# Kernel optimization log

Hardware: AMD Instinct MI355X
Metric: run time of the kernel (lower is better)

The kernel has to match this reference:

```python
import jax, jax.numpy as jnp
import numpy as np

TEMP = 0.07  # module hardcodes self.temp = 0.07 regardless of ctor arg
N, C = 8192, 256


def setup_inputs() -> dict:
    key = jax.random.key(0)
    kq, kk = jax.random.split(key)
    q = jax.random.normal(kq, (N, C), dtype=jnp.float32)
    k = jax.random.normal(kk, (N, C), dtype=jnp.float32)
    return {"q": q, "k": k}


def reference(q, k):
    # Original builds logits = [l_pos, l_neg_row] per sample i where
    # l_pos = q_i . k_i and l_neg_row = q_i . k_j for j != i, then applies
    # CrossEntropyLoss with label 0. That logits row is exactly a permutation
    # of the full similarity row sim[i, :] = q_i @ k.T (diagonal = positive),
    # so CE(logits/T, 0) == logsumexp(sim_i/T) - sim_ii/T. Single fused GEMM
    # + row-wise logsumexp, identical math and gradients.
    sim = jnp.matmul(q, k.T) / TEMP            # [N, N]
    pos = jnp.diagonal(sim)                    # [N]
    lse = jax.nn.logsumexp(sim, axis=1)        # [N]
    return jnp.mean(lse - pos)                 # scalar loss
```

## Files before the change

kernel.cpp:

```cpp
#include <hip/hip_runtime.h>
#include <stdint.h>


#define N_ROWS 8192
#define C_DIM  256
#define BN     64
#define SPLIT  16
#define JCOLS  (N_ROWS / SPLIT)
#define JTILES (JCOLS / BN)
#define RF     4
#define BLK_ROWS 256

typedef __attribute__((ext_vector_type(8))) _Float16 half8;
typedef __attribute__((ext_vector_type(4))) _Float16 half4;
typedef __attribute__((ext_vector_type(4))) float    f32x4;

#if __has_builtin(__builtin_amdgcn_exp2f)
#define EXP2(x) __builtin_amdgcn_exp2f(x)
#else
#define EXP2(x) exp2f(x)
#endif
#if __has_builtin(__builtin_amdgcn_logf)
#define LOG2(x) __builtin_amdgcn_logf(x)
#else
#define LOG2(x) log2f(x)
#endif

__device__ __forceinline__ void gload_lds16(const void* g, void* l) {
  __builtin_amdgcn_global_load_lds(
      (const __attribute__((address_space(1))) unsigned int*)g,
      (__attribute__((address_space(3))) unsigned int*)l, 16, 0, 0);
}

__global__ void cvt_kernel(const float* __restrict__ q, const float* __restrict__ k,
                           _Float16* __restrict__ qh, _Float16* __restrict__ kh,
                           float* __restrict__ pP) {
  const float QS = 20.60992915555663f;
  int i = blockIdx.x * 256 + threadIdx.x;
  float4 qv = ((const float4*)q)[i];
  float4 kv = ((const float4*)k)[i];
  half4 qo, ko;
  qo[0] = (_Float16)(qv.x * QS); qo[1] = (_Float16)(qv.y * QS);
  qo[2] = (_Float16)(qv.z * QS); qo[3] = (_Float16)(qv.w * QS);
  ko[0] = (_Float16)kv.x; ko[1] = (_Float16)kv.y;
  ko[2] = (_Float16)kv.z; ko[3] = (_Float16)kv.w;
  ((half4*)qh)[i] = qo;
  ((half4*)kh)[i] = ko;

  float d = (float)qo[0] * (float)ko[0];
  d = fmaf((float)qo[1], (float)ko[1], d);
  d = fmaf((float)qo[2], (float)ko[2], d);
  d = fmaf((float)qo[3], (float)ko[3], d);
#pragma unroll
  for (int off = 1; off < 64; off <<= 1) d += __shfl_xor(d, off);
  if ((threadIdx.x & 63) == 0) pP[i >> 6] = d;
}

__launch_bounds__(256, 2)
__global__ void sim_lse_kernel(const _Float16* __restrict__ qh,
                               const _Float16* __restrict__ kh,
                               float* __restrict__ pM,
                               float* __restrict__ pS) {
  __shared__ __align__(16) _Float16 kt[2 * BN * C_DIM];
  const int tid  = threadIdx.x;
  const int lane = tid & 63;
  const int wave = tid >> 6;
  const int l15  = lane & 15;
  const int lg   = lane >> 4;

  const int rb   = blockIdx.x;
  const int sp   = blockIdx.y;
  const int row0 = rb * BLK_ROWS + wave * 64;

  half8 a[RF][8];
#pragma unroll
  for (int rf = 0; rf < RF; ++rf) {
    const _Float16* qr = qh + (size_t)(row0 + rf * 16 + l15) * C_DIM + lg * 8;
#pragma unroll
    for (int f = 0; f < 8; ++f) a[rf][f] = *(const half8*)(qr + f * 32);
  }

  float M[RF][4], S[RF][4];
#pragma unroll
  for (int rf = 0; rf < RF; ++rf)
#pragma unroll
    for (int r = 0; r < 4; ++r) { M[rf][r] = -__builtin_inff(); S[rf][r] = 0.f; }

  int bbase[4];
#pragma unroll
  for (int cf = 0; cf < 4; ++cf) {
    int nl = cf * 16 + l15;
    bbase[cf] = nl * 512 + (((nl & 31) * 16) ^ (lg * 16));
  }

  const char* ksrc = (const char*)(kh + (size_t)sp * JCOLS * C_DIM);
  char* lds = (char*)kt;

#pragma unroll
  for (int it = 0; it < 8; ++it) {
    int linear = it * 4096 + tid * 16;
    int row = linear >> 9;
    int gc  = ((linear >> 4) & 31) ^ (row & 31);
    gload_lds16(ksrc + row * 512 + gc * 16, lds + linear);
  }

#pragma unroll 2
  for (int jt = 0; jt < JTILES; ++jt) {
    __syncthreads();
    const char* cur = lds + (jt & 1) * 32768;

    if (jt + 1 < JTILES) {
      const char* src = ksrc + (size_t)(jt + 1) * (BN * C_DIM * 2);
      char* nxt = lds + ((jt + 1) & 1) * 32768;
#pragma unroll
      for (int it = 0; it < 8; ++it) {
        int linear = it * 4096 + tid * 16;
        int row = linear >> 9;
        int gc  = ((linear >> 4) & 31) ^ (row & 31);
        gload_lds16(src + row * 512 + gc * 16, nxt + linear);
      }
    }

#pragma unroll
    for (int cp = 0; cp < 2; ++cp) {
      f32x4 acc0[RF], acc1[RF];
#pragma unroll
      for (int rf = 0; rf < RF; ++rf) {
        f32x4 z = {0.f, 0.f, 0.f, 0.f};
        acc0[rf] = z; acc1[rf] = z;
      }
      const int b0off = bbase[cp * 2];
      const int b1off = bbase[cp * 2 + 1];
#pragma unroll
      for (int ks = 0; ks < 8; ++ks) {
        half8 b0 = *(const half8*)(cur + (b0off ^ (ks * 64)));
        half8 b1 = *(const half8*)(cur + (b1off ^ (ks * 64)));
#pragma unroll
        for (int rf = 0; rf < RF; ++rf) {
          acc0[rf] = __builtin_amdgcn_mfma_f32_16x16x32_f16(a[rf][ks], b0, acc0[rf], 0, 0, 0);
          acc1[rf] = __builtin_amdgcn_mfma_f32_16x16x32_f16(a[rf][ks], b1, acc1[rf], 0, 0, 0);
        }
      }
#pragma unroll
      for (int rf = 0; rf < RF; ++rf)
#pragma unroll
        for (int r = 0; r < 4; ++r) {
          float v0 = acc0[rf][r], v1 = acc1[rf][r];
          float tmax  = fmaxf(v0, v1);
          float newM  = fmaxf(M[rf][r], tmax);
          float alpha = EXP2(M[rf][r] - newM);
          float p = EXP2(v0 - newM) + EXP2(v1 - newM);
          S[rf][r] = fmaf(S[rf][r], alpha, p);
          M[rf][r] = newM;
        }
    }
  }

#pragma unroll
  for (int rf = 0; rf < RF; ++rf)
#pragma unroll
    for (int r = 0; r < 4; ++r) {
#pragma unroll
      for (int off = 1; off < 16; off <<= 1) {
        float Mo = __shfl_xor(M[rf][r], off);
        float So = __shfl_xor(S[rf][r], off);
        float nm = fmaxf(M[rf][r], Mo);
        S[rf][r] = S[rf][r] * EXP2(M[rf][r] - nm) + So * EXP2(Mo - nm);
        M[rf][r] = nm;
      }
    }

  if (l15 == 0) {
#pragma unroll
    for (int rf = 0; rf < RF; ++rf)
#pragma unroll
      for (int r = 0; r < 4; ++r) {
        int grow = row0 + rf * 16 + lg * 4 + r;
        pM[(size_t)sp * N_ROWS + grow] = M[rf][r];
        pS[(size_t)sp * N_ROWS + grow] = S[rf][r];
      }
  }
}

__global__ void finish1_kernel(const float* __restrict__ pM, const float* __restrict__ pS,
                               const float* __restrict__ pP, float* __restrict__ pPart) {
  const int tid = threadIdx.x;
  const int r = blockIdx.x * 256 + tid;
  float m = -__builtin_inff();
#pragma unroll
  for (int s = 0; s < SPLIT; ++s) m = fmaxf(m, pM[s * N_ROWS + r]);
  float ssum = 0.f;
#pragma unroll
  for (int s = 0; s < SPLIT; ++s)
    ssum = fmaf(pS[s * N_ROWS + r], EXP2(pM[s * N_ROWS + r] - m), ssum);
  float accl = (m + LOG2(ssum)) - pP[r];
#pragma unroll
  for (int off = 1; off < 64; off <<= 1) accl += __shfl_xor(accl, off);
  __shared__ float wsum[4];
  if ((tid & 63) == 0) wsum[tid >> 6] = accl;
  __syncthreads();
  if (tid == 0)
    pPart[blockIdx.x] = wsum[0] + wsum[1] + wsum[2] + wsum[3];
}

__global__ void finish2_kernel(const float* __restrict__ pPart, float* __restrict__ out) {
  const int tid = threadIdx.x;
  float v = (tid < 32) ? pPart[tid] : 0.f;
#pragma unroll
  for (int off = 1; off < 64; off <<= 1) v += __shfl_xor(v, off);
  if (tid == 0)
    out[0] = v * (0.69314718055994531f / (float)N_ROWS);
}

extern "C" void kernel_launch(void* const* d_in, const int* in_sizes, int n_in,
                              void* d_out, int out_size, void* d_ws, size_t ws_size,
                              hipStream_t stream) {
  const float* q = (const float*)d_in[0];
  const float* k = (const float*)d_in[1];
  float* out = (float*)d_out;
  char* ws = (char*)d_ws;

  _Float16* qh = (_Float16*)ws;
  _Float16* kh = (_Float16*)(ws + (size_t)N_ROWS * C_DIM * 2);
  float* pM = (float*)(ws + (size_t)N_ROWS * C_DIM * 4);
  float* pS = pM + SPLIT * N_ROWS;
  float* pP = pS + SPLIT * N_ROWS;
  float* pPart = pP + N_ROWS;

  cvt_kernel<<<dim3(N_ROWS * C_DIM / 4 / 256), dim3(256), 0, stream>>>(q, k, qh, kh, pP);
  sim_lse_kernel<<<dim3(N_ROWS / BLK_ROWS, SPLIT), dim3(256), 0, stream>>>(qh, kh, pM, pS);
  finish1_kernel<<<dim3(N_ROWS / 256), dim3(256), 0, stream>>>(pM, pS, pP, pPart);
  finish2_kernel<<<dim3(1), dim3(64), 0, stream>>>(pPart, out);
}
```

Measured before the change: 137.9 us.

## Switch similarity GEMM to 32x32x16 MFMA with 128-row blocks and split 8

Replaces the 16x16x32 MFMA tiling (4 row fragments per wave, 64 rows) with 32x32x16 MFMA (32 rows per wave, 128-row blocks) and halves the column split from 16 to 8, flattening the grid to 1D with split as the fastest index. The goal is higher MFMA throughput per LDS read and fewer partial M/S results. The trade-off is less K-tile reuse per block (128 rows instead of 256), so the K matrix is re-read from global/LDS more often. Blocks sharing a row block are launched adjacently, which may help L2 locality. Row mapping for the 32x32 output layout is rewritten for the final stores.

```diff
diff --git a/kernel.cpp b/kernel.cpp
--- a/kernel.cpp
+++ b/kernel.cpp
@@ -5,15 +5,14 @@
 #define N_ROWS 8192
 #define C_DIM  256
 #define BN     64
-#define SPLIT  16
+#define SPLIT  8
 #define JCOLS  (N_ROWS / SPLIT)
 #define JTILES (JCOLS / BN)
-#define RF     4
-#define BLK_ROWS 256
-
-typedef __attribute__((ext_vector_type(8))) _Float16 half8;
-typedef __attribute__((ext_vector_type(4))) _Float16 half4;
-typedef __attribute__((ext_vector_type(4))) float    f32x4;
+#define BLK_ROWS 128
+
+typedef __attribute__((ext_vector_type(8)))  _Float16 half8;
+typedef __attribute__((ext_vector_type(4)))  _Float16 half4;
+typedef __attribute__((ext_vector_type(16))) float    f32x16;
 
 #if __has_builtin(__builtin_amdgcn_exp2f)
 #define EXP2(x) __builtin_amdgcn_exp2f(x)
@@ -65,33 +64,27 @@
   const int tid  = threadIdx.x;
   const int lane = tid & 63;
   const int wave = tid >> 6;
-  const int l15  = lane & 15;
-  const int lg   = lane >> 4;
-
-  const int rb   = blockIdx.x;
-  const int sp   = blockIdx.y;
-  const int row0 = rb * BLK_ROWS + wave * 64;
-
-  half8 a[RF][8];
-#pragma unroll
-  for (int rf = 0; rf < RF; ++rf) {
-    const _Float16* qr = qh + (size_t)(row0 + rf * 16 + l15) * C_DIM + lg * 8;
-#pragma unroll
-    for (int f = 0; f < 8; ++f) a[rf][f] = *(const half8*)(qr + f * 32);
-  }
-
-  float M[RF][4], S[RF][4];
-#pragma unroll
-  for (int rf = 0; rf < RF; ++rf)
-#pragma unroll
-    for (int r = 0; r < 4; ++r) { M[rf][r] = -__builtin_inff(); S[rf][r] = 0.f; }
-
-  int bbase[4];
-#pragma unroll
-  for (int cf = 0; cf < 4; ++cf) {
-    int nl = cf * 16 + l15;
-    bbase[cf] = nl * 512 + (((nl & 31) * 16) ^ (lg * 16));
-  }
+  const int r    = lane & 31;
+  const int hi   = lane >> 5;
+
+  const int bid  = blockIdx.x;
+  const int sp   = bid & (SPLIT - 1);
+  const int rb   = bid >> 3;
+  const int row0 = rb * BLK_ROWS + wave * 32;
+
+  half8 a[16];
+  {
+    const _Float16* qr = qh + (size_t)(row0 + r) * C_DIM + hi * 8;
+#pragma unroll
+    for (int ks = 0; ks < 16; ++ks) a[ks] = *(const half8*)(qr + ks * 16);
+  }
+
+  float M[16], S[16];
+#pragma unroll
+  for (int j = 0; j < 16; ++j) { M[j] = -__builtin_inff(); S[j] = 0.f; }
+
+  const int bb0 = r * 512 + ((hi ^ r) << 4);
+  const int bb1 = bb0 + 32 * 512;
 
   const char* ksrc = (const char*)(kh + (size_t)sp * JCOLS * C_DIM);
   char* lds = (char*)kt;
@@ -104,7 +97,6 @@
     gload_lds16(ksrc + row * 512 + gc * 16, lds + linear);
   }
 
-#pragma unroll 2
   for (int jt = 0; jt < JTILES; ++jt) {
     __syncthreads();
     const char* cur = lds + (jt & 1) * 32768;
@@ -121,64 +113,49 @@
       }
     }
 
-#pragma unroll
-    for (int cp = 0; cp < 2; ++cp) {
-      f32x4 acc0[RF], acc1[RF];
-#pragma unroll
-      for (int rf = 0; rf < RF; ++rf) {
-        f32x4 z = {0.f, 0.f, 0.f, 0.f};
-        acc0[rf] = z; acc1[rf] = z;
-      }
-      const int b0off = bbase[cp * 2];
-      const int b1off = bbase[cp * 2 + 1];
-#pragma unroll
-      for (int ks = 0; ks < 8; ++ks) {
-        half8 b0 = *(const half8*)(cur + (b0off ^ (ks * 64)));
-        half8 b1 = *(const half8*)(cur + (b1off ^ (ks * 64)));
-#pragma unroll
-        for (int rf = 0; rf < RF; ++rf) {
-          acc0[rf] = __builtin_amdgcn_mfma_f32_16x16x32_f16(a[rf][ks], b0, acc0[rf], 0, 0, 0);
-          acc1[rf] = __builtin_amdgcn_mfma_f32_16x16x32_f16(a[rf][ks], b1, acc1[rf], 0, 0, 0);
-        }
-      }
-#pragma unroll
-      for (int rf = 0; rf < RF; ++rf)
-#pragma unroll
-        for (int r = 0; r < 4; ++r) {
-          float v0 = acc0[rf][r], v1 = acc1[rf][r];
-          float tmax  = fmaxf(v0, v1);
-          float newM  = fmaxf(M[rf][r], tmax);
-          float alpha = EXP2(M[rf][r] - newM);
-          float p = EXP2(v0 - newM) + EXP2(v1 - newM);
-          S[rf][r] = fmaf(S[rf][r], alpha, p);
-          M[rf][r] = newM;
-        }
-    }
-  }
-
-#pragma unroll
-  for (int rf = 0; rf < RF; ++rf)
-#pragma unroll
-    for (int r = 0; r < 4; ++r) {
-#pragma unroll
-      for (int off = 1; off < 16; off <<= 1) {
-        float Mo = __shfl_xor(M[rf][r], off);
-        float So = __shfl_xor(S[rf][r], off);
-        float nm = fmaxf(M[rf][r], Mo);
-        S[rf][r] = S[rf][r] * EXP2(M[rf][r] - nm) + So * EXP2(Mo - nm);
-        M[rf][r] = nm;
-      }
-    }
-
-  if (l15 == 0) {
-#pragma unroll
-    for (int rf = 0; rf < RF; ++rf)
-#pragma unroll
-      for (int r = 0; r < 4; ++r) {
-        int grow = row0 + rf * 16 + lg * 4 + r;
-        pM[(size_t)sp * N_ROWS + grow] = M[rf][r];
-        pS[(size_t)sp * N_ROWS + grow] = S[rf][r];
-      }
+    f32x16 acc0, acc1;
+#pragma unroll
+    for (int j = 0; j < 16; ++j) { acc0[j] = 0.f; acc1[j] = 0.f; }
+
+#pragma unroll
+    for (int ks = 0; ks < 16; ++ks) {
+      half8 b0 = *(const half8*)(cur + (bb0 ^ (ks * 32)));
+      half8 b1 = *(const half8*)(cur + (bb1 ^ (ks * 32)));
+      acc0 = __builtin_amdgcn_mfma_f32_32x32x16_f16(a[ks], b0, acc0, 0, 0, 0);
+      acc1 = __builtin_amdgcn_mfma_f32_32x32x16_f16(a[ks], b1, acc1, 0, 0, 0);
+    }
+
+#pragma unroll
+    for (int j = 0; j < 16; ++j) {
+      float v0 = acc0[j], v1 = acc1[j];
+      float tmax  = fmaxf(v0, v1);
+      float newM  = fmaxf(M[j], tmax);
+      float alpha = EXP2(M[j] - newM);
+      float p = EXP2(v0 - newM) + EXP2(v1 - newM);
+      S[j] = fmaf(S[j], alpha, p);
+      M[j] = newM;
+    }
+  }
+
+#pragma unroll
+  for (int j = 0; j < 16; ++j) {
+#pragma unroll
+    for (int off = 1; off < 32; off <<= 1) {
+      float Mo = __shfl_xor(M[j], off);
+      float So = __shfl_xor(S[j], off);
+      float nm = fmaxf(M[j], Mo);
+      S[j] = S[j] * EXP2(M[j] - nm) + So * EXP2(Mo - nm);
+      M[j] = nm;
+    }
+  }
+
+  if ((lane & 31) == 0) {
+#pragma unroll
+    for (int j = 0; j < 16; ++j) {
+      int grow = row0 + (j & 3) + 8 * (j >> 2) + 4 * hi;
+      pM[(size_t)sp * N_ROWS + grow] = M[j];
+      pS[(size_t)sp * N_ROWS + grow] = S[j];
+    }
   }
 }
 
@@ -228,7 +205,7 @@
   float* pPart = pP + N_ROWS;
 
   cvt_kernel<<<dim3(N_ROWS * C_DIM / 4 / 256), dim3(256), 0, stream>>>(q, k, qh, kh, pP);
-  sim_lse_kernel<<<dim3(N_ROWS / BLK_ROWS, SPLIT), dim3(256), 0, stream>>>(qh, kh, pM, pS);
+  sim_lse_kernel<<<dim3((N_ROWS / BLK_ROWS) * SPLIT), dim3(256), 0, stream>>>(qh, kh, pM, pS);
   finish1_kernel<<<dim3(N_ROWS / 256), dim3(256), 0, stream>>>(pM, pS, pP, pPart);
   finish2_kernel<<<dim3(1), dim3(64), 0, stream>>>(pPart, out);
 }
```

After: 116.0 us. 1.19x faster.
